# Kernel optimization log

Hardware: AMD Instinct MI355X
Metric: run time of the kernel (lower is better)

## Reference

```python
import jax, jax.numpy as jnp
import numpy as np

D_MODEL = 256
N_HEAD = 8


def setup_inputs() -> dict:
    key = jax.random.key(0)
    ks = jax.random.split(key, 9)
    B, S, D = 2, 2048, D_MODEL
    s = 1.0 / np.sqrt(D)
    return {
        "x": jax.random.normal(ks[0], (B, S, D), dtype=jnp.float32),
        "wq": jax.random.uniform(ks[1], (D, D), jnp.float32, -s, s),
        "bq": jax.random.uniform(ks[2], (D,), jnp.float32, -s, s),
        "wk": jax.random.uniform(ks[3], (D, D), jnp.float32, -s, s),
        "bk": jax.random.uniform(ks[4], (D,), jnp.float32, -s, s),
        "wv": jax.random.uniform(ks[5], (D, D), jnp.float32, -s, s),
        "bv": jax.random.uniform(ks[6], (D,), jnp.float32, -s, s),
        "wc": jax.random.uniform(ks[7], (D, D), jnp.float32, -s, s),
        "bc": jax.random.uniform(ks[8], (D,), jnp.float32, -s, s),
    }


def _split_heads(t):
    # [B, S, D] -> [B, H, S, D/H]
    B, S, D = t.shape
    return t.reshape(B, S, N_HEAD, D // N_HEAD).transpose(0, 2, 1, 3)


def reference(x, wq, bq, wk, bk, wv, bv, wc, bc):
    q = _split_heads(x @ wq.T + bq)
    k = _split_heads(x @ wk.T + bk)
    v = _split_heads(x @ wv.T + bv)
    d_head = q.shape[-1]
    # full [B, H, S, S] score matrix, as in the original (non-fused)
    score = jnp.einsum("bhqd,bhkd->bhqk", q, k) / jnp.sqrt(jnp.float32(d_head))
    attn = jax.nn.softmax(score, axis=-1)
    out = jnp.einsum("bhqk,bhkd->bhqd", attn, v)
    B, H, S, Dh = out.shape
    out = out.transpose(0, 2, 1, 3).reshape(B, S, H * Dh)
    out = out @ wc.T + bc
    attention = jnp.mean(attn, axis=1)  # [B, S, S]
    return (out, attention)
```

## Files before the change

kernel.cpp:

```cpp
#include <hip/hip_runtime.h>
#include <hip/hip_bf16.h>


#define B_   2
#define S_   2048
#define D_   256
#define H_   8
#define DH_  32
#define NROW (B_*S_)
#define KSPLIT 4
#define KKEYS (S_/KSPLIT)

typedef __attribute__((ext_vector_type(8))) short bf16x8;
typedef __attribute__((ext_vector_type(4))) float f32x4;

__device__ __forceinline__ f32x4 mfma_bf16(bf16x8 a, bf16x8 b, f32x4 c) {
    return __builtin_amdgcn_mfma_f32_16x16x32_bf16(a, b, c, 0, 0, 0);
}

__device__ __forceinline__ float fast_exp2(float x) {
    return __builtin_amdgcn_exp2f(x);
}

__device__ __forceinline__ unsigned short f2bf_bits(float v) {
    __hip_bfloat16 h = __float2bfloat16(v);
    return *reinterpret_cast<unsigned short*>(&h);
}

__device__ __forceinline__ size_t fragidx(int m, int k) {
    return (size_t)(m >> 4) * 4096 + (k >> 5) * 512 + ((k >> 3) & 3) * 128
           + (m & 15) * 8 + (k & 7);
}

__global__ void split_all(const float4* __restrict__ x,
                          const float4* __restrict__ wq, const float4* __restrict__ wk,
                          const float4* __restrict__ wv, const float4* __restrict__ wc,
                          ushort4* __restrict__ xh, ushort4* __restrict__ xl,
                          ushort4* __restrict__ wqh, ushort4* __restrict__ wql,
                          ushort4* __restrict__ wkh, ushort4* __restrict__ wkl,
                          ushort4* __restrict__ wvh, ushort4* __restrict__ wvl,
                          ushort4* __restrict__ wch, ushort4* __restrict__ wcl) {
    int i = blockIdx.x * 256 + threadIdx.x;
    const float4* src; ushort4 *ph, *pl; int off;
    if (i < 262144) { src = x; ph = xh; pl = xl; off = i; }
    else {
        int j = i - 262144;
        int rg = j >> 14; off = j & 16383;
        if (rg == 0)      { src = wq; ph = wqh; pl = wql; }
        else if (rg == 1) { src = wk; ph = wkh; pl = wkl; }
        else if (rg == 2) { src = wv; ph = wvh; pl = wvl; }
        else              { src = wc; ph = wch; pl = wcl; }
    }
    float4 v = src[off];
    float vv[4] = {v.x, v.y, v.z, v.w};
    ushort4 hb, lb;
    unsigned short* hp = (unsigned short*)&hb;
    unsigned short* lp = (unsigned short*)&lb;
    for (int c = 0; c < 4; c++) {
        __hip_bfloat16 h = __float2bfloat16(vv[c]);
        hp[c] = *reinterpret_cast<unsigned short*>(&h);
        lp[c] = f2bf_bits(vv[c] - __bfloat162float(h));
    }
    int m = off >> 6, k = (off & 63) * 4;
    size_t fi = fragidx(m, k);
    ph[fi >> 2] = hb;
    pl[fi >> 2] = lb;
}

__global__ __launch_bounds__(256) void qkv_gemm(
    const __hip_bfloat16* __restrict__ xh, const __hip_bfloat16* __restrict__ xl,
    const __hip_bfloat16* __restrict__ w0h, const __hip_bfloat16* __restrict__ w0l,
    const __hip_bfloat16* __restrict__ w1h, const __hip_bfloat16* __restrict__ w1l,
    const __hip_bfloat16* __restrict__ w2h, const __hip_bfloat16* __restrict__ w2l,
    const float* __restrict__ bq, const float* __restrict__ bk, const float* __restrict__ bvv,
    __hip_bfloat16* __restrict__ Qf, __hip_bfloat16* __restrict__ Kf,
    __hip_bfloat16* __restrict__ Vf)
{
    int z = blockIdx.z;
    const __hip_bfloat16* wh = (z==0) ? w0h : (z==1) ? w1h : w2h;
    const __hip_bfloat16* wl = (z==0) ? w0l : (z==1) ? w1l : w2l;
    const float* bias = (z==0) ? bq : (z==1) ? bk : bvv;
    const float sv = (z==0) ? 0.17677669529663687f * 1.4426950408889634f : 1.0f;

    int tid = threadIdx.x;
    int w = tid >> 6, lid = tid & 63, quad = lid >> 4, l15 = lid & 15;
    int row0 = blockIdx.x * 64 + (w >> 1) * 32;
    int col0 = blockIdx.y * 64 + (w & 1) * 32;

    f32x4 acc[2][2] = {};
#pragma unroll
    for (int k0 = 0; k0 < 256; k0 += 32) {
        bf16x8 ah[2], al[2], bh[2], bl[2];
        for (int mi = 0; mi < 2; mi++) {
            size_t ro = (size_t)((row0 + mi * 16) >> 4) * 4096 + (k0 >> 5) * 512 + lid * 8;
            ah[mi] = *(const bf16x8*)(xh + ro);
            al[mi] = *(const bf16x8*)(xl + ro);
        }
        for (int ni = 0; ni < 2; ni++) {
            size_t co = (size_t)((col0 + ni * 16) >> 4) * 4096 + (k0 >> 5) * 512 + lid * 8;
            bh[ni] = *(const bf16x8*)(wh + co);
            bl[ni] = *(const bf16x8*)(wl + co);
        }
        for (int mi = 0; mi < 2; mi++)
            for (int ni = 0; ni < 2; ni++) {
                acc[mi][ni] = mfma_bf16(ah[mi], bh[ni], acc[mi][ni]);
                acc[mi][ni] = mfma_bf16(ah[mi], bl[ni], acc[mi][ni]);
                acc[mi][ni] = mfma_bf16(al[mi], bh[ni], acc[mi][ni]);
            }
    }
    for (int mi = 0; mi < 2; mi++)
        for (int ni = 0; ni < 2; ni++) {
            int col = col0 + ni * 16 + l15;
            int h = col >> 5, dh = col & 31;
            float bvl = bias[col];
            for (int r = 0; r < 4; r++) {
                int row = row0 + mi * 16 + quad * 4 + r;
                int b = row >> 11, s = row & 2047;
                __hip_bfloat16 o = __float2bfloat16((acc[mi][ni][r] + bvl) * sv);
                size_t bh_base = (size_t)(b * H_ + h) * (S_ * DH_);
                if (z == 2) {
                    int oo = s & 31;
                    int slot = ((oo & 15) >> 2) * 8 + ((oo >> 4) << 2) + (oo & 3);
                    Vf[bh_base + (s >> 5) * 1024 + (dh >> 4) * 512
                       + (slot >> 3) * 128 + (dh & 15) * 8 + (slot & 7)] = o;
                } else {
                    size_t idx = bh_base + (s >> 4) * 512 + (dh >> 3) * 128
                                 + (s & 15) * 8 + (dh & 7);
                    if (z == 0) Qf[idx] = o; else Kf[idx] = o;
                }
            }
        }
}

__global__ __launch_bounds__(256) void attn_flash(
    const __hip_bfloat16* __restrict__ Qf, const __hip_bfloat16* __restrict__ Kf,
    const __hip_bfloat16* __restrict__ Vf,
    __hip_bfloat16* __restrict__ cth, __hip_bfloat16* __restrict__ ctl,
    float* __restrict__ invL)
{
    __shared__ float sO[KSPLIT][16][33];
    __shared__ float sL[KSPLIT][16];
    int f = blockIdx.x;
    int g = (f & 7) * 256 + (f >> 3);
    int qt = g & 127;
    int h = (g >> 7) & 7;
    int b = g >> 10;
    int q0 = qt * 16;
    int tid = threadIdx.x, w = tid >> 6, lid = tid & 63, quad = lid >> 4, l15 = lid & 15;
    size_t bh_base = (size_t)(b * H_ + h) * (S_ * DH_);
    const __hip_bfloat16* Qp = Qf + bh_base + (q0 >> 4) * 512 + lid * 8;
    const __hip_bfloat16* Kp = Kf + bh_base + lid * 8;
    const __hip_bfloat16* Vp = Vf + bh_base + lid * 8;
    bf16x8 qf = *(const bf16x8*)Qp;
    f32x4 zacc = {};
    f32x4 oacc[2] = {};
    float lp0 = 0.f, lp1 = 0.f;

    int kbeg = w * KKEYS;
    bf16x8 kf0 = *(const bf16x8*)(Kp + (kbeg >> 4) * 512);
    bf16x8 kf1 = *(const bf16x8*)(Kp + (kbeg >> 4) * 512 + 512);
    bf16x8 vf0 = *(const bf16x8*)(Vp + (kbeg >> 5) * 1024);
    bf16x8 vf1 = *(const bf16x8*)(Vp + (kbeg >> 5) * 1024 + 512);

#pragma unroll 2
    for (int k0 = kbeg; k0 < kbeg + KKEYS; k0 += 32) {
        bf16x8 ck0 = kf0, ck1 = kf1, cv0 = vf0, cv1 = vf1;
        int kn = (k0 + 32 < kbeg + KKEYS) ? k0 + 32 : kbeg;
        kf0 = *(const bf16x8*)(Kp + (kn >> 4) * 512);
        kf1 = *(const bf16x8*)(Kp + (kn >> 4) * 512 + 512);
        vf0 = *(const bf16x8*)(Vp + (kn >> 5) * 1024);
        vf1 = *(const bf16x8*)(Vp + (kn >> 5) * 1024 + 512);

        __builtin_amdgcn_s_setprio(1);
        f32x4 c0 = mfma_bf16(ck0, qf, zacc);
        f32x4 c1 = mfma_bf16(ck1, qf, zacc);
        __builtin_amdgcn_s_setprio(0);
        float e0[4], e1[4];
        for (int r = 0; r < 4; r++) {
            e0[r] = fast_exp2(c0[r]);
            e1[r] = fast_exp2(c1[r]);
        }
        lp0 += e0[0] + e0[1] + e0[2] + e0[3];
        lp1 += e1[0] + e1[1] + e1[2] + e1[3];
        union { bf16x8 v; __hip_bfloat162 h2[4]; } pu;
        pu.h2[0] = __float22bfloat162_rn(make_float2(e0[0], e0[1]));
        pu.h2[1] = __float22bfloat162_rn(make_float2(e0[2], e0[3]));
        pu.h2[2] = __float22bfloat162_rn(make_float2(e1[0], e1[1]));
        pu.h2[3] = __float22bfloat162_rn(make_float2(e1[2], e1[3]));
        __builtin_amdgcn_s_setprio(1);
        oacc[0] = mfma_bf16(cv0, pu.v, oacc[0]);
        oacc[1] = mfma_bf16(cv1, pu.v, oacc[1]);
        __builtin_amdgcn_s_setprio(0);
    }
    float lp = lp0 + lp1;
    lp += __shfl_xor(lp, 16);
    lp += __shfl_xor(lp, 32);

    for (int r = 0; r < 4; r++) {
        sO[w][l15][quad * 4 + r]      = oacc[0][r];
        sO[w][l15][16 + quad * 4 + r] = oacc[1][r];
    }
    if (lid < 16) sL[w][lid] = lp;
    __syncthreads();

    int d = tid & 31, q = tid >> 5;
#pragma unroll
    for (int qq = q; qq < 16; qq += 8) {
        float l = sL[0][qq] + sL[1][qq] + sL[2][qq] + sL[3][qq];
        float o = sO[0][qq][d] + sO[1][qq][d] + sO[2][qq][d] + sO[3][qq][d];
        float inv = 1.0f / l;
        float val = o * inv;
        size_t fi = fragidx(b * S_ + q0 + qq, h * DH_ + d);
        __hip_bfloat16 hv = __float2bfloat16(val);
        cth[fi] = hv;
        ctl[fi] = __float2bfloat16(val - __bfloat162float(hv));
        if (d == 0) invL[(b * H_ + h) * S_ + q0 + qq] = inv;
    }
}

__global__ __launch_bounds__(256) void attn_out(
    const __hip_bfloat16* __restrict__ Qf, const __hip_bfloat16* __restrict__ Kf,
    const float* __restrict__ invL,
    const __hip_bfloat16* __restrict__ ch, const __hip_bfloat16* __restrict__ cl,
    const __hip_bfloat16* __restrict__ wh, const __hip_bfloat16* __restrict__ wl,
    const float* __restrict__ bias,
    float* __restrict__ attn, float* __restrict__ out)
{
    __shared__ float invbuf[H_ * 16];
    int bid = blockIdx.x;
    int tid = threadIdx.x, w = tid >> 6, lid = tid & 63, quad = lid >> 4, l15 = lid & 15;

    if (bid < 256) {
        int row0 = (bid & 63) * 64 + (w >> 1) * 32;
        int col0 = (bid >> 6) * 64 + (w & 1) * 32;

        f32x4 acc[2][2] = {};
#pragma unroll
        for (int k0 = 0; k0 < 256; k0 += 32) {
            bf16x8 ah[2], al[2], bh[2], bl[2];
            for (int mi = 0; mi < 2; mi++) {
                size_t ro = (size_t)((row0 + mi * 16) >> 4) * 4096 + (k0 >> 5) * 512 + lid * 8;
                ah[mi] = *(const bf16x8*)(ch + ro);
                al[mi] = *(const bf16x8*)(cl + ro);
            }
            for (int ni = 0; ni < 2; ni++) {
                size_t co = (size_t)((col0 + ni * 16) >> 4) * 4096 + (k0 >> 5) * 512 + lid * 8;
                bh[ni] = *(const bf16x8*)(wh + co);
                bl[ni] = *(const bf16x8*)(wl + co);
            }
            for (int mi = 0; mi < 2; mi++)
                for (int ni = 0; ni < 2; ni++) {
                    acc[mi][ni] = mfma_bf16(ah[mi], bh[ni], acc[mi][ni]);
                    acc[mi][ni] = mfma_bf16(ah[mi], bl[ni], acc[mi][ni]);
                    acc[mi][ni] = mfma_bf16(al[mi], bh[ni], acc[mi][ni]);
                }
        }
        for (int mi = 0; mi < 2; mi++)
            for (int ni = 0; ni < 2; ni++) {
                int col = col0 + ni * 16 + l15;
                float bvl = bias[col];
                for (int r = 0; r < 4; r++) {
                    int row = row0 + mi * 16 + quad * 4 + r;
                    out[(size_t)row * 256 + col] = acc[mi][ni][r] + bvl;
                }
            }
    } else {
        int f2 = bid - 256;
        int g = (f2 & 7) * 256 + (f2 >> 3);
        int qy = g & 127, kx = (g >> 7) & 7, b = g >> 10;
        int q0 = qy * 16;
        int k0 = kx * 256 + w * 64;
        if (tid < 128) {
            int h = tid >> 4, r = tid & 15;
            invbuf[tid] = invL[(b * H_ + h) * S_ + q0 + r] * 0.125f;
        }
        __syncthreads();
        f32x4 zacc = {};
        float psum[4][4] = {};
        size_t bh0 = (size_t)b * H_ * (S_ * DH_);
        size_t qoff = (size_t)(q0 >> 4) * 512 + lid * 8;
        size_t koff = (size_t)(k0 >> 4) * 512 + lid * 8;

        bf16x8 qcur = *(const bf16x8*)(Qf + bh0 + qoff);
        bf16x8 kcur0 = *(const bf16x8*)(Kf + bh0 + koff);
        bf16x8 kcur1 = *(const bf16x8*)(Kf + bh0 + koff + 512);
        bf16x8 kcur2 = *(const bf16x8*)(Kf + bh0 + koff + 1024);
        bf16x8 kcur3 = *(const bf16x8*)(Kf + bh0 + koff + 1536);

#pragma unroll 2
        for (int h = 0; h < H_; h++) {
            int hn = (h < H_ - 1) ? h + 1 : h;
            size_t nb = bh0 + (size_t)hn * (S_ * DH_);
            bf16x8 qn = *(const bf16x8*)(Qf + nb + qoff);
            bf16x8 kn0 = *(const bf16x8*)(Kf + nb + koff);
            bf16x8 kn1 = *(const bf16x8*)(Kf + nb + koff + 512);
            bf16x8 kn2 = *(const bf16x8*)(Kf + nb + koff + 1024);
            bf16x8 kn3 = *(const bf16x8*)(Kf + nb + koff + 1536);

            float il[4];
            for (int r = 0; r < 4; r++) il[r] = invbuf[h * 16 + quad * 4 + r];

            __builtin_amdgcn_s_setprio(1);
            f32x4 c0 = mfma_bf16(qcur, kcur0, zacc);
            f32x4 c1 = mfma_bf16(qcur, kcur1, zacc);
            f32x4 c2 = mfma_bf16(qcur, kcur2, zacc);
            f32x4 c3 = mfma_bf16(qcur, kcur3, zacc);
            __builtin_amdgcn_s_setprio(0);
            for (int r = 0; r < 4; r++) {
                psum[0][r] += fast_exp2(c0[r]) * il[r];
                psum[1][r] += fast_exp2(c1[r]) * il[r];
                psum[2][r] += fast_exp2(c2[r]) * il[r];
                psum[3][r] += fast_exp2(c3[r]) * il[r];
            }
            qcur = qn;
            kcur0 = kn0; kcur1 = kn1; kcur2 = kn2; kcur3 = kn3;
        }
        for (int nt = 0; nt < 4; nt++)
            for (int r = 0; r < 4; r++)
                attn[(size_t)(b * S_ + q0 + quad * 4 + r) * S_ + k0 + nt * 16 + l15] =
                    psum[nt][r];
    }
}

extern "C" void kernel_launch(void* const* d_in, const int* in_sizes, int n_in,
                              void* d_out, int out_size, void* d_ws, size_t ws_size,
                              hipStream_t stream) {
    const float* x  = (const float*)d_in[0];
    const float* wq = (const float*)d_in[1];
    const float* bq = (const float*)d_in[2];
    const float* wk = (const float*)d_in[3];
    const float* bk = (const float*)d_in[4];
    const float* wv = (const float*)d_in[5];
    const float* bv = (const float*)d_in[6];
    const float* wc = (const float*)d_in[7];
    const float* bc = (const float*)d_in[8];

    char* ws = (char*)d_ws;
    const size_t MB = 1u << 20;
    const size_t KB128 = 128u * 1024u;
    __hip_bfloat16* xh  = (__hip_bfloat16*)(ws + 0 * MB);
    __hip_bfloat16* xl  = (__hip_bfloat16*)(ws + 2 * MB);
    __hip_bfloat16* wqh = (__hip_bfloat16*)(ws + 4 * MB + 0 * KB128);
    __hip_bfloat16* wql = (__hip_bfloat16*)(ws + 4 * MB + 1 * KB128);
    __hip_bfloat16* wkh = (__hip_bfloat16*)(ws + 4 * MB + 2 * KB128);
    __hip_bfloat16* wkl = (__hip_bfloat16*)(ws + 4 * MB + 3 * KB128);
    __hip_bfloat16* wvh = (__hip_bfloat16*)(ws + 4 * MB + 4 * KB128);
    __hip_bfloat16* wvl = (__hip_bfloat16*)(ws + 4 * MB + 5 * KB128);
    __hip_bfloat16* wch = (__hip_bfloat16*)(ws + 4 * MB + 6 * KB128);
    __hip_bfloat16* wcl = (__hip_bfloat16*)(ws + 4 * MB + 7 * KB128);
    __hip_bfloat16* Qfb = (__hip_bfloat16*)(ws + 5 * MB);
    __hip_bfloat16* Kfb = (__hip_bfloat16*)(ws + 7 * MB);
    __hip_bfloat16* Vfb = (__hip_bfloat16*)(ws + 9 * MB);
    __hip_bfloat16* cth = (__hip_bfloat16*)(ws + 11 * MB);
    __hip_bfloat16* ctl = (__hip_bfloat16*)(ws + 13 * MB);
    float* invL  = (float*)(ws + 15 * MB);

    float* outp  = (float*)d_out;
    float* attnp = outp + (size_t)NROW * D_;

    hipLaunchKernelGGL(split_all, dim3(1280), dim3(256), 0, stream,
                       (const float4*)x, (const float4*)wq, (const float4*)wk,
                       (const float4*)wv, (const float4*)wc,
                       (ushort4*)xh, (ushort4*)xl,
                       (ushort4*)wqh, (ushort4*)wql, (ushort4*)wkh, (ushort4*)wkl,
                       (ushort4*)wvh, (ushort4*)wvl, (ushort4*)wch, (ushort4*)wcl);

    hipLaunchKernelGGL(qkv_gemm, dim3(NROW / 64, 4, 3), dim3(256), 0, stream,
                       xh, xl, wqh, wql, wkh, wkl, wvh, wvl, bq, bk, bv, Qfb, Kfb, Vfb);

    hipLaunchKernelGGL(attn_flash, dim3(2048), dim3(256), 0, stream,
                       Qfb, Kfb, Vfb, cth, ctl, invL);

    hipLaunchKernelGGL(attn_out, dim3(256 + 2048), dim3(256), 0, stream,
                       Qfb, Kfb, invL, cth, ctl, wch, wcl, bc, attnp, outp);
}
```

Before: 134.2 us.

## Process 32 queries per block in flash and attention-map kernels to reuse K/V

Each block in both attention kernels now handles two 16-query tiles, so every loaded K/V fragment feeds twice as many MFMAs, and the grids are halved. The explicit software prefetch of the next K/V (and next head's Q/K) is removed in favour of plain in-loop loads. This cuts global/L2 traffic per query and block count, but raises register pressure, lowers parallelism to 1024 blocks, and drops the manual load pipelining.

```diff
diff --git a/kernel.cpp b/kernel.cpp
--- a/kernel.cpp
+++ b/kernel.cpp
@@ -138,74 +138,79 @@
     __hip_bfloat16* __restrict__ cth, __hip_bfloat16* __restrict__ ctl,
     float* __restrict__ invL)
 {
-    __shared__ float sO[KSPLIT][16][33];
-    __shared__ float sL[KSPLIT][16];
+    __shared__ float sO[KSPLIT][32][33];
+    __shared__ float sL[KSPLIT][32];
     int f = blockIdx.x;
-    int g = (f & 7) * 256 + (f >> 3);
-    int qt = g & 127;
-    int h = (g >> 7) & 7;
-    int b = g >> 10;
-    int q0 = qt * 16;
+    int g = (f & 7) * 128 + (f >> 3);
+    int qt = g & 63;
+    int h = (g >> 6) & 7;
+    int b = g >> 9;
+    int q0 = qt * 32;
     int tid = threadIdx.x, w = tid >> 6, lid = tid & 63, quad = lid >> 4, l15 = lid & 15;
     size_t bh_base = (size_t)(b * H_ + h) * (S_ * DH_);
     const __hip_bfloat16* Qp = Qf + bh_base + (q0 >> 4) * 512 + lid * 8;
     const __hip_bfloat16* Kp = Kf + bh_base + lid * 8;
     const __hip_bfloat16* Vp = Vf + bh_base + lid * 8;
-    bf16x8 qf = *(const bf16x8*)Qp;
+    bf16x8 qfA = *(const bf16x8*)Qp;
+    bf16x8 qfB = *(const bf16x8*)(Qp + 512);
     f32x4 zacc = {};
-    f32x4 oacc[2] = {};
-    float lp0 = 0.f, lp1 = 0.f;
+    f32x4 oacc[2][2] = {};
+    float lpA = 0.f, lpB = 0.f;
 
     int kbeg = w * KKEYS;
-    bf16x8 kf0 = *(const bf16x8*)(Kp + (kbeg >> 4) * 512);
-    bf16x8 kf1 = *(const bf16x8*)(Kp + (kbeg >> 4) * 512 + 512);
-    bf16x8 vf0 = *(const bf16x8*)(Vp + (kbeg >> 5) * 1024);
-    bf16x8 vf1 = *(const bf16x8*)(Vp + (kbeg >> 5) * 1024 + 512);
-
 #pragma unroll 2
     for (int k0 = kbeg; k0 < kbeg + KKEYS; k0 += 32) {
-        bf16x8 ck0 = kf0, ck1 = kf1, cv0 = vf0, cv1 = vf1;
-        int kn = (k0 + 32 < kbeg + KKEYS) ? k0 + 32 : kbeg;
-        kf0 = *(const bf16x8*)(Kp + (kn >> 4) * 512);
-        kf1 = *(const bf16x8*)(Kp + (kn >> 4) * 512 + 512);
-        vf0 = *(const bf16x8*)(Vp + (kn >> 5) * 1024);
-        vf1 = *(const bf16x8*)(Vp + (kn >> 5) * 1024 + 512);
+        bf16x8 kf0 = *(const bf16x8*)(Kp + (k0 >> 4) * 512);
+        bf16x8 kf1 = *(const bf16x8*)(Kp + (k0 >> 4) * 512 + 512);
+        bf16x8 vf0 = *(const bf16x8*)(Vp + (k0 >> 5) * 1024);
+        bf16x8 vf1 = *(const bf16x8*)(Vp + (k0 >> 5) * 1024 + 512);
 
         __builtin_amdgcn_s_setprio(1);
-        f32x4 c0 = mfma_bf16(ck0, qf, zacc);
-        f32x4 c1 = mfma_bf16(ck1, qf, zacc);
+        f32x4 cA0 = mfma_bf16(kf0, qfA, zacc);
+        f32x4 cA1 = mfma_bf16(kf1, qfA, zacc);
+        f32x4 cB0 = mfma_bf16(kf0, qfB, zacc);
+        f32x4 cB1 = mfma_bf16(kf1, qfB, zacc);
         __builtin_amdgcn_s_setprio(0);
-        float e0[4], e1[4];
+        float eA0[4], eA1[4], eB0[4], eB1[4];
         for (int r = 0; r < 4; r++) {
-            e0[r] = fast_exp2(c0[r]);
-            e1[r] = fast_exp2(c1[r]);
-        }
-        lp0 += e0[0] + e0[1] + e0[2] + e0[3];
-        lp1 += e1[0] + e1[1] + e1[2] + e1[3];
-        union { bf16x8 v; __hip_bfloat162 h2[4]; } pu;
-        pu.h2[0] = __float22bfloat162_rn(make_float2(e0[0], e0[1]));
-        pu.h2[1] = __float22bfloat162_rn(make_float2(e0[2], e0[3]));
-        pu.h2[2] = __float22bfloat162_rn(make_float2(e1[0], e1[1]));
-        pu.h2[3] = __float22bfloat162_rn(make_float2(e1[2], e1[3]));
+            eA0[r] = fast_exp2(cA0[r]);
+            eA1[r] = fast_exp2(cA1[r]);
+            eB0[r] = fast_exp2(cB0[r]);
+            eB1[r] = fast_exp2(cB1[r]);
+        }
+        lpA += eA0[0] + eA0[1] + eA0[2] + eA0[3] + eA1[0] + eA1[1] + eA1[2] + eA1[3];
+        lpB += eB0[0] + eB0[1] + eB0[2] + eB0[3] + eB1[0] + eB1[1] + eB1[2] + eB1[3];
+        union { bf16x8 v; __hip_bfloat162 h2[4]; } puA, puB;
+        puA.h2[0] = __float22bfloat162_rn(make_float2(eA0[0], eA0[1]));
+        puA.h2[1] = __float22bfloat162_rn(make_float2(eA0[2], eA0[3]));
+        puA.h2[2] = __float22bfloat162_rn(make_float2(eA1[0], eA1[1]));
+        puA.h2[3] = __float22bfloat162_rn(make_float2(eA1[2], eA1[3]));
+        puB.h2[0] = __float22bfloat162_rn(make_float2(eB0[0], eB0[1]));
+        puB.h2[1] = __float22bfloat162_rn(make_float2(eB0[2], eB0[3]));
+        puB.h2[2] = __float22bfloat162_rn(make_float2(eB1[0], eB1[1]));
+        puB.h2[3] = __float22bfloat162_rn(make_float2(eB1[2], eB1[3]));
         __builtin_amdgcn_s_setprio(1);
-        oacc[0] = mfma_bf16(cv0, pu.v, oacc[0]);
-        oacc[1] = mfma_bf16(cv1, pu.v, oacc[1]);
+        oacc[0][0] = mfma_bf16(vf0, puA.v, oacc[0][0]);
+        oacc[0][1] = mfma_bf16(vf1, puA.v, oacc[0][1]);
+        oacc[1][0] = mfma_bf16(vf0, puB.v, oacc[1][0]);
+        oacc[1][1] = mfma_bf16(vf1, puB.v, oacc[1][1]);
         __builtin_amdgcn_s_setprio(0);
     }
-    float lp = lp0 + lp1;
-    lp += __shfl_xor(lp, 16);
-    lp += __shfl_xor(lp, 32);
-
-    for (int r = 0; r < 4; r++) {
-        sO[w][l15][quad * 4 + r]      = oacc[0][r];
-        sO[w][l15][16 + quad * 4 + r] = oacc[1][r];
-    }
-    if (lid < 16) sL[w][lid] = lp;
+    lpA += __shfl_xor(lpA, 16);
+    lpA += __shfl_xor(lpA, 32);
+    lpB += __shfl_xor(lpB, 16);
+    lpB += __shfl_xor(lpB, 32);
+
+    for (int qg = 0; qg < 2; qg++)
+        for (int dh2 = 0; dh2 < 2; dh2++)
+            for (int r = 0; r < 4; r++)
+                sO[w][qg * 16 + l15][dh2 * 16 + quad * 4 + r] = oacc[qg][dh2][r];
+    if (lid < 16) { sL[w][lid] = lpA; sL[w][16 + lid] = lpB; }
     __syncthreads();
 
     int d = tid & 31, q = tid >> 5;
 #pragma unroll
-    for (int qq = q; qq < 16; qq += 8) {
+    for (int qq = q; qq < 32; qq += 8) {
         float l = sL[0][qq] + sL[1][qq] + sL[2][qq] + sL[3][qq];
         float o = sO[0][qq][d] + sO[1][qq][d] + sO[2][qq][d] + sO[3][qq][d];
         float inv = 1.0f / l;
@@ -226,7 +231,7 @@
     const float* __restrict__ bias,
     float* __restrict__ attn, float* __restrict__ out)
 {
-    __shared__ float invbuf[H_ * 16];
+    __shared__ float invbuf[H_ * 32];
     int bid = blockIdx.x;
     int tid = threadIdx.x, w = tid >> 6, lid = tid & 63, quad = lid >> 4, l15 = lid & 15;
 
@@ -266,59 +271,60 @@
             }
     } else {
         int f2 = bid - 256;
-        int g = (f2 & 7) * 256 + (f2 >> 3);
-        int qy = g & 127, kx = (g >> 7) & 7, b = g >> 10;
-        int q0 = qy * 16;
+        int g = (f2 & 7) * 128 + (f2 >> 3);
+        int qy = g & 63, kx = (g >> 6) & 7, b = g >> 9;
+        int q0 = qy * 32;
         int k0 = kx * 256 + w * 64;
-        if (tid < 128) {
-            int h = tid >> 4, r = tid & 15;
-            invbuf[tid] = invL[(b * H_ + h) * S_ + q0 + r] * 0.125f;
-        }
+        invbuf[tid] = invL[(b * H_ + (tid >> 5)) * S_ + q0 + (tid & 31)] * 0.125f;
         __syncthreads();
         f32x4 zacc = {};
-        float psum[4][4] = {};
+        float psum[2][4][4] = {};
         size_t bh0 = (size_t)b * H_ * (S_ * DH_);
         size_t qoff = (size_t)(q0 >> 4) * 512 + lid * 8;
         size_t koff = (size_t)(k0 >> 4) * 512 + lid * 8;
 
-        bf16x8 qcur = *(const bf16x8*)(Qf + bh0 + qoff);
-        bf16x8 kcur0 = *(const bf16x8*)(Kf + bh0 + koff);
-        bf16x8 kcur1 = *(const bf16x8*)(Kf + bh0 + koff + 512);
-        bf16x8 kcur2 = *(const bf16x8*)(Kf + bh0 + koff + 1024);
-        bf16x8 kcur3 = *(const bf16x8*)(Kf + bh0 + koff + 1536);
-
 #pragma unroll 2
         for (int h = 0; h < H_; h++) {
-            int hn = (h < H_ - 1) ? h + 1 : h;
-            size_t nb = bh0 + (size_t)hn * (S_ * DH_);
-            bf16x8 qn = *(const bf16x8*)(Qf + nb + qoff);
-            bf16x8 kn0 = *(const bf16x8*)(Kf + nb + koff);
-            bf16x8 kn1 = *(const bf16x8*)(Kf + nb + koff + 512);
-            bf16x8 kn2 = *(const bf16x8*)(Kf + nb + koff + 1024);
-            bf16x8 kn3 = *(const bf16x8*)(Kf + nb + koff + 1536);
-
-            float il[4];
-            for (int r = 0; r < 4; r++) il[r] = invbuf[h * 16 + quad * 4 + r];
+            size_t nb = bh0 + (size_t)h * (S_ * DH_);
+            bf16x8 qfA = *(const bf16x8*)(Qf + nb + qoff);
+            bf16x8 qfB = *(const bf16x8*)(Qf + nb + qoff + 512);
+            bf16x8 kf0 = *(const bf16x8*)(Kf + nb + koff);
+            bf16x8 kf1 = *(const bf16x8*)(Kf + nb + koff + 512);
+            bf16x8 kf2 = *(const bf16x8*)(Kf + nb + koff + 1024);
+            bf16x8 kf3 = *(const bf16x8*)(Kf + nb + koff + 1536);
+
+            float ilA[4], ilB[4];
+            for (int r = 0; r < 4; r++) {
+                ilA[r] = invbuf[h * 32 + quad * 4 + r];
+                ilB[r] = invbuf[h * 32 + 16 + quad * 4 + r];
+            }
 
             __builtin_amdgcn_s_setprio(1);
-            f32x4 c0 = mfma_bf16(qcur, kcur0, zacc);
-            f32x4 c1 = mfma_bf16(qcur, kcur1, zacc);
-            f32x4 c2 = mfma_bf16(qcur, kcur2, zacc);
-            f32x4 c3 = mfma_bf16(qcur, kcur3, zacc);
+            f32x4 cA0 = mfma_bf16(qfA, kf0, zacc);
+            f32x4 cA1 = mfma_bf16(qfA, kf1, zacc);
+            f32x4 cA2 = mfma_bf16(qfA, kf2, zacc);
+            f32x4 cA3 = mfma_bf16(qfA, kf3, zacc);
+            f32x4 cB0 = mfma_bf16(qfB, kf0, zacc);
+            f32x4 cB1 = mfma_bf16(qfB, kf1, zacc);
+            f32x4 cB2 = mfma_bf16(qfB, kf2, zacc);
+            f32x4 cB3 = mfma_bf16(qfB, kf3, zacc);
             __builtin_amdgcn_s_setprio(0);
             for (int r = 0; r < 4; r++) {
-                psum[0][r] += fast_exp2(c0[r]) * il[r];
-                psum[1][r] += fast_exp2(c1[r]) * il[r];
-                psum[2][r] += fast_exp2(c2[r]) * il[r];
-                psum[3][r] += fast_exp2(c3[r]) * il[r];
-            }
-            qcur = qn;
-            kcur0 = kn0; kcur1 = kn1; kcur2 = kn2; kcur3 = kn3;
-        }
-        for (int nt = 0; nt < 4; nt++)
-            for (int r = 0; r < 4; r++)
-                attn[(size_t)(b * S_ + q0 + quad * 4 + r) * S_ + k0 + nt * 16 + l15] =
-                    psum[nt][r];
+                psum[0][0][r] += fast_exp2(cA0[r]) * ilA[r];
+                psum[0][1][r] += fast_exp2(cA1[r]) * ilA[r];
+                psum[0][2][r] += fast_exp2(cA2[r]) * ilA[r];
+                psum[0][3][r] += fast_exp2(cA3[r]) * ilA[r];
+                psum[1][0][r] += fast_exp2(cB0[r]) * ilB[r];
+                psum[1][1][r] += fast_exp2(cB1[r]) * ilB[r];
+                psum[1][2][r] += fast_exp2(cB2[r]) * ilB[r];
+                psum[1][3][r] += fast_exp2(cB3[r]) * ilB[r];
+            }
+        }
+        for (int qg = 0; qg < 2; qg++)
+            for (int nt = 0; nt < 4; nt++)
+                for (int r = 0; r < 4; r++)
+                    attn[(size_t)(b * S_ + q0 + qg * 16 + quad * 4 + r) * S_
+                         + k0 + nt * 16 + l15] = psum[qg][nt][r];
     }
 }
 
@@ -368,9 +374,9 @@
     hipLaunchKernelGGL(qkv_gemm, dim3(NROW / 64, 4, 3), dim3(256), 0, stream,
                        xh, xl, wqh, wql, wkh, wkl, wvh, wvl, bq, bk, bv, Qfb, Kfb, Vfb);
 
-    hipLaunchKernelGGL(attn_flash, dim3(2048), dim3(256), 0, stream,
+    hipLaunchKernelGGL(attn_flash, dim3(1024), dim3(256), 0, stream,
                        Qfb, Kfb, Vfb, cth, ctl, invL);
 
-    hipLaunchKernelGGL(attn_out, dim3(256 + 2048), dim3(256), 0, stream,
+    hipLaunchKernelGGL(attn_out, dim3(256 + 1024), dim3(256), 0, stream,
                        Qfb, Kfb, invL, cth, ctl, wch, wcl, bc, attnp, outp);
 }
```

After: 127.0 us, median of 2. 1.06x faster.
